# Optimization experiments

Measured on AMD Instinct MI355X. Metric: run time of the kernel, lower is better.

The kernel has to match this reference:

```python
import jax, jax.numpy as jnp
import numpy as np

B, S, D, E = 4, 4096, 1024, 8

def setup_inputs() -> dict:
    key = jax.random.key(0)
    k1, k2, k3, k4, k5 = jax.random.split(key, 5)
    scale = 1.0 / np.sqrt(D)
    return {
        "x": jax.random.normal(k1, (B, S, D), dtype=jnp.float32),
        "Wg": jax.random.normal(k2, (D, D), dtype=jnp.float32) * scale,   # gate Linear(D, D)
        "bg": jnp.zeros((D,), dtype=jnp.float32),
        "We": jax.random.normal(k3, (E, D, D), dtype=jnp.float32) * scale,  # per-expert Linear(D, D)
        "be": jnp.zeros((E, D), dtype=jnp.float32),
    }

def reference(x, Wg, bg, We, be):
    # gating network: Linear + Softmax over last dim (size D, per the original module)
    probs = jax.nn.softmax(x @ Wg + bg, axis=-1)           # [B,S,D]
    idx = jnp.argmax(probs, axis=-1)                        # [B,S], values in [0, D)
    p = jnp.take_along_axis(probs, idx[..., None], axis=-1)[..., 0]  # top-1 gate prob
    e_idx = idx % We.shape[0]                               # map argmax to expert id
    # run every expert densely, then select routed expert per token (top-1 switch routing)
    h = jax.nn.relu(jnp.einsum('bsd,edf->besf', x, We) + be[None, :, None, :])  # [B,E,S,D]
    onehot = jax.nn.one_hot(e_idx, We.shape[0], dtype=x.dtype)                   # [B,S,E]
    out = jnp.einsum('besf,bse->bsf', h, onehot) * p[..., None]                  # [B,S,D]
    return out
```

## Files before the change

kernel.cpp:

```cpp
#include <hip/hip_runtime.h>
#include <stdint.h>
#include <stddef.h>

#define TOK    16384
#define DDIM   1024
#define NEXP   8
#define BMT    128
#define RB_MAX 136
#define MARGIN 2.5e-2f
#define AMBIG_CAP 4096
#define BK     64

typedef __bf16 bf16x8 __attribute__((ext_vector_type(8)));
typedef float  f32x4  __attribute__((ext_vector_type(4)));
typedef unsigned short u16x8 __attribute__((ext_vector_type(8)));

__device__ __forceinline__ unsigned short f2bf(float f) {
    unsigned int u = __float_as_uint(f);
    u += 0x7fff + ((u >> 16) & 1);
    return (unsigned short)(u >> 16);
}

__device__ __forceinline__ void gload_lds16(const void* g, void* l) {
    __builtin_amdgcn_global_load_lds(
        (const __attribute__((address_space(1))) unsigned int*)g,
        (__attribute__((address_space(3))) unsigned int*)l, 16, 0, 0);
}

__global__ __launch_bounds__(256) void cvt_x(
    const float* __restrict__ x, unsigned short* __restrict__ xbf)
{
    const size_t t = ((size_t)blockIdx.x * 256 + threadIdx.x) * 8;
    const float4 v0 = *(const float4*)(x + t);
    const float4 v1 = *(const float4*)(x + t + 4);
    const float vv[8] = {v0.x, v0.y, v0.z, v0.w, v1.x, v1.y, v1.z, v1.w};
    u16x8 hh;
#pragma unroll
    for (int j = 0; j < 8; j++) hh[j] = f2bf(vv[j]);
    *(u16x8*)(xbf + t) = hh;
}

__global__ __launch_bounds__(256) void transpose_mat(
    const float* __restrict__ src0, unsigned short* __restrict__ dst0)
{
    __shared__ float tile[32][33];
    const int e  = blockIdx.z;
    const int k0 = blockIdx.x * 32;
    const int n0 = blockIdx.y * 32;
    const int tx = threadIdx.x;
    const int ty = threadIdx.y;
    const float* src = src0 + (size_t)e * DDIM * DDIM;
    unsigned short* dst = dst0 + (size_t)e * DDIM * DDIM;
#pragma unroll
    for (int r = 0; r < 4; r++)
        tile[ty + r * 8][tx] = src[(size_t)(k0 + ty + r * 8) * DDIM + n0 + tx];
    __syncthreads();
#pragma unroll
    for (int r = 0; r < 4; r++)
        dst[(size_t)(n0 + ty + r * 8) * DDIM + k0 + tx] = f2bf(tile[tx][ty + r * 8]);
}

__global__ __launch_bounds__(256) void transpose_f32(
    const float* __restrict__ src, float* __restrict__ dst)
{
    __shared__ float tile[32][33];
    const int k0 = blockIdx.x * 32;
    const int n0 = blockIdx.y * 32;
    const int tx = threadIdx.x;
    const int ty = threadIdx.y;
#pragma unroll
    for (int r = 0; r < 4; r++)
        tile[ty + r * 8][tx] = src[(size_t)(k0 + ty + r * 8) * DDIM + n0 + tx];
    __syncthreads();
#pragma unroll
    for (int r = 0; r < 4; r++)
        dst[(size_t)(n0 + ty + r * 8) * DDIM + k0 + tx] = tile[tx][ty + r * 8];
}

__global__ __launch_bounds__(256) void gating_mfma(
    const unsigned short* __restrict__ xbf,
    const unsigned short* __restrict__ WgT,
    const float* __restrict__ bg, float* __restrict__ logits)
{
    __shared__ unsigned short Asm[128 * BK];
    __shared__ unsigned short Bsm[128 * BK];
    const int rb = blockIdx.x;
    const int nb = blockIdx.y;
    const int tid  = threadIdx.x;
    const int lane = tid & 63;
    const int wave = tid >> 6;
    const int q    = lane >> 4;
    const int m16  = lane & 15;
    const int wrow = (wave & 1) * 64;
    const int wcol = (wave >> 1) * 64;

    const unsigned short* Ag = xbf + (size_t)rb * 128 * DDIM;
    const unsigned short* Bg = WgT + (size_t)nb * 128 * DDIM;

    const unsigned short* pa[4];
    const unsigned short* pb[4];
#pragma unroll
    for (int i = 0; i < 4; i++) {
        const int idx = tid + i * 256;
        const int r = idx >> 3;
        const int c = idx & 7;
        const int g = (c ^ (r & 7)) * 8;
        pa[i] = Ag + (size_t)r * DDIM + g;
        pb[i] = Bg + (size_t)r * DDIM + g;
    }

    f32x4 acc[4][4];
#pragma unroll
    for (int i = 0; i < 4; i++)
#pragma unroll
        for (int j = 0; j < 4; j++) acc[i][j] = (f32x4){0.f, 0.f, 0.f, 0.f};

    for (int k0 = 0; k0 < DDIM; k0 += BK) {
#pragma unroll
        for (int i = 0; i < 4; i++) {
            gload_lds16(pa[i] + k0, &Asm[(tid + i * 256) * 8]);
            gload_lds16(pb[i] + k0, &Bsm[(tid + i * 256) * 8]);
        }
        __syncthreads();
#pragma unroll
        for (int s = 0; s < 2; s++) {
            const int cs = (((s << 2) + q) ^ (m16 & 7)) << 3;
            bf16x8 af[4], bfr[4];
#pragma unroll
            for (int i = 0; i < 4; i++)
                af[i] = *(const bf16x8*)&Asm[(wrow + i * 16 + m16) * BK + cs];
#pragma unroll
            for (int j = 0; j < 4; j++)
                bfr[j] = *(const bf16x8*)&Bsm[(wcol + j * 16 + m16) * BK + cs];
#pragma unroll
            for (int i = 0; i < 4; i++)
#pragma unroll
                for (int j = 0; j < 4; j++)
                    acc[i][j] = __builtin_amdgcn_mfma_f32_16x16x32_bf16(
                        af[i], bfr[j], acc[i][j], 0, 0, 0);
        }
        __syncthreads();
    }

    float bgv[4];
#pragma unroll
    for (int j = 0; j < 4; j++) bgv[j] = bg[nb * 128 + wcol + j * 16 + m16];
#pragma unroll
    for (int i = 0; i < 4; i++)
#pragma unroll
        for (int r = 0; r < 4; r++) {
            const int row = rb * 128 + wrow + i * 16 + q * 4 + r;
#pragma unroll
            for (int j = 0; j < 4; j++) {
                const int col = nb * 128 + wcol + j * 16 + m16;
                logits[(size_t)row * DDIM + col] = acc[i][j][r] + bgv[j];
            }
        }
}

__global__ __launch_bounds__(256) void row_stats(
    const float* __restrict__ logits, float* __restrict__ pout,
    int* __restrict__ eout, float* __restrict__ rmax_a, float* __restrict__ s_a,
    int* __restrict__ ambig, int* __restrict__ n_ambig)
{
    const int row  = blockIdx.x * 4 + (threadIdx.x >> 6);
    const int lane = threadIdx.x & 63;
    const float* L = logits + (size_t)row * DDIM;
    float vals[16];
#pragma unroll
    for (int i = 0; i < 4; i++)
        *(float4*)&vals[i * 4] = *(const float4*)&L[lane * 16 + i * 4];
    float m = vals[0]; int mi = lane * 16;
#pragma unroll
    for (int i = 1; i < 16; i++)
        if (vals[i] > m) { m = vals[i]; mi = lane * 16 + i; }
    for (int off = 32; off > 0; off >>= 1) {
        float ov = __shfl_down(m, off, 64);
        int   oi = __shfl_down(mi, off, 64);
        if (ov > m || (ov == m && oi < mi)) { m = ov; mi = oi; }
    }
    m  = __shfl(m, 0, 64);
    mi = __shfl(mi, 0, 64);
    float s = 0.f;
    int   c = 0;
#pragma unroll
    for (int i = 0; i < 16; i++) {
        s += expf(vals[i] - m);
        if (vals[i] >= m - MARGIN) c++;
    }
    for (int off = 32; off > 0; off >>= 1) {
        s += __shfl_xor(s, off, 64);
        c += __shfl_xor(c, off, 64);
    }
    if (lane == 0) {
        pout[row] = 1.0f / s;
        eout[row] = mi & (NEXP - 1);
        rmax_a[row] = m;
        s_a[row] = s;
        if (c > 1) {
            int k = atomicAdd(n_ambig, 1);
            if (k < AMBIG_CAP) ambig[k] = row;
        }
    }
}

__global__ __launch_bounds__(64) void fixup(
    const float* __restrict__ logits, const float* __restrict__ x,
    const float* __restrict__ WgTf, const float* __restrict__ bg,
    const float* __restrict__ rmax_a, const float* __restrict__ s_a,
    const int* __restrict__ ambig, const int* __restrict__ n_ambig,
    int* __restrict__ eout, float* __restrict__ pout)
{
    int n = *n_ambig; if (n > AMBIG_CAP) n = AMBIG_CAP;
    if ((int)blockIdx.x >= n) return;
    const int row  = ambig[blockIdx.x];
    const int lane = threadIdx.x;
    const float rmax = rmax_a[row];
    const float* L = logits + (size_t)row * DDIM;
    __shared__ int scnt;
    __shared__ int scol[32];
    if (lane == 0) scnt = 0;
    __syncthreads();
    for (int j = lane; j < DDIM; j += 64)
        if (L[j] >= rmax - MARGIN) {
            int k = atomicAdd(&scnt, 1);
            if (k < 32) scol[k] = j;
        }
    __syncthreads();
    int ncand = scnt < 32 ? scnt : 32;
    double bestv = -1e300; int bestc = DDIM;
    for (int cidx = 0; cidx < ncand; cidx++) {
        const int col = scol[cidx];
        const float* Wcol = WgTf + (size_t)col * DDIM;
        double s = 0.0;
        for (int k = lane; k < DDIM; k += 64)
            s += (double)x[(size_t)row * DDIM + k] * (double)Wcol[k];
        for (int off = 32; off > 0; off >>= 1) s += __shfl_down(s, off, 64);
        s = __shfl(s, 0, 64);
        s += (double)bg[col];
        if (s > bestv || (s == bestv && col < bestc)) { bestv = s; bestc = col; }
    }
    if (lane == 0) {
        eout[row] = bestc & (NEXP - 1);
        pout[row] = expf(L[bestc] - rmax) / s_a[row];
    }
}

__global__ __launch_bounds__(256) void histo(const int* __restrict__ eout,
                                             int* __restrict__ cnt)
{
    __shared__ int h[NEXP];
    if (threadIdx.x < NEXP) h[threadIdx.x] = 0;
    __syncthreads();
    const int t = blockIdx.x * 256 + threadIdx.x;
    if (t < TOK) atomicAdd(&h[eout[t]], 1);
    __syncthreads();
    if (threadIdx.x < NEXP) atomicAdd(&cnt[threadIdx.x], h[threadIdx.x]);
}

__global__ __launch_bounds__(256) void compute_offsets(
    const int* __restrict__ cnt, int* __restrict__ start,
    int* __restrict__ blk_expert)
{
    const int tid = threadIdx.x;
    int st[NEXP + 1];
    int total = 0;
#pragma unroll
    for (int e = 0; e < NEXP; e++) {
        st[e] = total;
        total += ((cnt[e] + BMT - 1) / BMT) * BMT;
    }
    st[NEXP] = total;
    if (tid <= NEXP) start[tid] = st[tid];
    if (tid < RB_MAX) {
        const int s = tid * BMT;
        int ex = -1;
#pragma unroll
        for (int e = 0; e < NEXP; e++)
            if (s >= st[e] && s < st[e + 1]) ex = e;
        blk_expert[tid] = ex;
    }
}

__global__ __launch_bounds__(256) void assign_slots(
    const int* __restrict__ eout, const int* __restrict__ start,
    int* __restrict__ cursor, int* __restrict__ row_of_slot)
{
    __shared__ int h[NEXP];
    __shared__ int base[NEXP];
    const int tid = threadIdx.x;
    if (tid < NEXP) h[tid] = 0;
    __syncthreads();
    const int t = blockIdx.x * 256 + tid;
    int e = 0, lr = 0;
    if (t < TOK) {
        e = eout[t];
        lr = atomicAdd(&h[e], 1);
    }
    __syncthreads();
    if (tid < NEXP && h[tid] > 0)
        base[tid] = atomicAdd(&cursor[tid], h[tid]);
    __syncthreads();
    if (t < TOK)
        row_of_slot[start[e] + base[e] + lr] = t;
}

__global__ __launch_bounds__(256) void expert_gemm(
    const unsigned short* __restrict__ xbf, const unsigned short* __restrict__ WeT,
    const float* __restrict__ be, const float* __restrict__ p,
    const int* __restrict__ row_of_slot, const int* __restrict__ blk_expert,
    float* __restrict__ out)
{
    __shared__ unsigned short Asm[128 * BK];
    __shared__ unsigned short Bsm[128 * BK];
    __shared__ int rs[128];
    const int rb = blockIdx.x;
    const int nb = blockIdx.y;
    const int e = blk_expert[rb];
    if (e < 0) return;

    const int tid  = threadIdx.x;
    const int lane = tid & 63;
    const int wave = tid >> 6;
    const int q    = lane >> 4;
    const int m16  = lane & 15;
    const int wrow = (wave & 1) * 64;
    const int wcol = (wave >> 1) * 64;

    if (tid < 128) rs[tid] = row_of_slot[rb * 128 + tid];
    __syncthreads();

    const unsigned short* Bglob = WeT + (size_t)e * DDIM * DDIM + (size_t)nb * 128 * DDIM;

    const unsigned short* pa[4];
    const unsigned short* pb[4];
#pragma unroll
    for (int i = 0; i < 4; i++) {
        const int idx = tid + i * 256;
        const int r = idx >> 3;
        const int c = idx & 7;
        const int g = (c ^ (r & 7)) * 8;
        int tr = rs[r]; if (tr < 0) tr = 0;
        pa[i] = xbf + (size_t)tr * DDIM + g;
        pb[i] = Bglob + (size_t)r * DDIM + g;
    }

    f32x4 acc[4][4];
#pragma unroll
    for (int i = 0; i < 4; i++)
#pragma unroll
        for (int j = 0; j < 4; j++) acc[i][j] = (f32x4){0.f, 0.f, 0.f, 0.f};

    for (int k0 = 0; k0 < DDIM; k0 += BK) {
#pragma unroll
        for (int i = 0; i < 4; i++) {
            gload_lds16(pa[i] + k0, &Asm[(tid + i * 256) * 8]);
            gload_lds16(pb[i] + k0, &Bsm[(tid + i * 256) * 8]);
        }
        __syncthreads();
#pragma unroll
        for (int s = 0; s < 2; s++) {
            const int cs = (((s << 2) + q) ^ (m16 & 7)) << 3;
            bf16x8 af[4], bfr[4];
#pragma unroll
            for (int i = 0; i < 4; i++)
                af[i] = *(const bf16x8*)&Asm[(wrow + i * 16 + m16) * BK + cs];
#pragma unroll
            for (int j = 0; j < 4; j++)
                bfr[j] = *(const bf16x8*)&Bsm[(wcol + j * 16 + m16) * BK + cs];
#pragma unroll
            for (int i = 0; i < 4; i++)
#pragma unroll
                for (int j = 0; j < 4; j++)
                    acc[i][j] = __builtin_amdgcn_mfma_f32_16x16x32_bf16(
                        af[i], bfr[j], acc[i][j], 0, 0, 0);
        }
        __syncthreads();
    }

    float bev[4];
#pragma unroll
    for (int j = 0; j < 4; j++) bev[j] = be[e * DDIM + nb * 128 + wcol + j * 16 + m16];
#pragma unroll
    for (int i = 0; i < 4; i++)
#pragma unroll
        for (int r = 0; r < 4; r++) {
            const int t = rs[wrow + i * 16 + q * 4 + r];
            if (t < 0) continue;
            const float pv = p[t];
#pragma unroll
            for (int j = 0; j < 4; j++) {
                const int n = nb * 128 + wcol + j * 16 + m16;
                float v = acc[i][j][r] + bev[j];
                v = v > 0.f ? v : 0.f;
                out[(size_t)t * DDIM + n] = v * pv;
            }
        }
}

extern "C" void kernel_launch(void* const* d_in, const int* in_sizes, int n_in,
                              void* d_out, int out_size, void* d_ws, size_t ws_size,
                              hipStream_t stream)
{
    const float* x  = (const float*)d_in[0];
    const float* Wg = (const float*)d_in[1];
    const float* bg = (const float*)d_in[2];
    const float* We = (const float*)d_in[3];
    const float* be = (const float*)d_in[4];
    float* out = (float*)d_out;

    char* ws = (char*)d_ws;
    float* logits = (float*)ws;                 ws += (size_t)TOK * DDIM * 4;
    unsigned short* WeT = (unsigned short*)ws;  ws += (size_t)NEXP * DDIM * DDIM * 2;
    unsigned short* WgT = (unsigned short*)ws;  ws += (size_t)DDIM * DDIM * 2;
    float* WgTf = (float*)ws;                   ws += (size_t)DDIM * DDIM * 4;
    unsigned short* xbf = (unsigned short*)ws;  ws += (size_t)TOK * DDIM * 2;
    float* p = (float*)ws;                      ws += (size_t)TOK * 4;
    int* e_arr = (int*)ws;                      ws += (size_t)TOK * 4;
    float* rmax_a = (float*)ws;                 ws += (size_t)TOK * 4;
    float* s_a = (float*)ws;                    ws += (size_t)TOK * 4;
    int* row_of_slot = (int*)ws;                ws += (size_t)RB_MAX * BMT * 4;
    int* cnt = (int*)ws;                        ws += NEXP * 4;
    int* cursor = (int*)ws;                     ws += NEXP * 4;
    int* start = (int*)ws;                      ws += (NEXP + 1) * 4;
    int* blk_expert = (int*)ws;                 ws += RB_MAX * 4;
    int* ambig = (int*)ws;                      ws += AMBIG_CAP * 4;
    int* n_ambig = (int*)ws;                    ws += 4;

    hipMemsetAsync(cnt, 0, NEXP * 4, stream);
    hipMemsetAsync(cursor, 0, NEXP * 4, stream);
    hipMemsetAsync(n_ambig, 0, 4, stream);
    hipMemsetAsync(row_of_slot, 0xFF, (size_t)RB_MAX * BMT * 4, stream);

    cvt_x<<<TOK * DDIM / (256 * 8), 256, 0, stream>>>(x, xbf);
    transpose_mat<<<dim3(32, 32, 1), dim3(32, 8), 0, stream>>>(Wg, WgT);
    transpose_f32<<<dim3(32, 32), dim3(32, 8), 0, stream>>>(Wg, WgTf);
    transpose_mat<<<dim3(32, 32, NEXP), dim3(32, 8), 0, stream>>>(We, WeT);
    gating_mfma<<<dim3(TOK / 128, DDIM / 128), 256, 0, stream>>>(xbf, WgT, bg, logits);
    row_stats<<<TOK / 4, 256, 0, stream>>>(logits, p, e_arr, rmax_a, s_a, ambig, n_ambig);
    fixup<<<AMBIG_CAP, 64, 0, stream>>>(logits, x, WgTf, bg, rmax_a, s_a, ambig, n_ambig, e_arr, p);
    histo<<<TOK / 256, 256, 0, stream>>>(e_arr, cnt);
    compute_offsets<<<1, 256, 0, stream>>>(cnt, start, blk_expert);
    assign_slots<<<TOK / 256, 256, 0, stream>>>(e_arr, start, cursor, row_of_slot);
    expert_gemm<<<dim3(RB_MAX, DDIM / 128), 256, 0, stream>>>(
        xbf, WeT, be, p, row_of_slot, blk_expert, out);
}
```

Before: 326.1 us.

## Double-buffer GEMM K loop with 256x256 tiles and 512-thread blocks

```diff
diff --git a/kernel.cpp b/kernel.cpp
--- a/kernel.cpp
+++ b/kernel.cpp
@@ -5,11 +5,12 @@
 #define TOK    16384
 #define DDIM   1024
 #define NEXP   8
-#define BMT    128
-#define RB_MAX 136
+#define BMT    256
+#define RB_MAX 72
 #define MARGIN 2.5e-2f
 #define AMBIG_CAP 4096
-#define BK     64
+#define BK     32
+#define KT_N   (DDIM / BK)
 
 typedef __bf16 bf16x8 __attribute__((ext_vector_type(8)));
 typedef float  f32x4  __attribute__((ext_vector_type(4)));
@@ -26,6 +27,33 @@
         (const __attribute__((address_space(1))) unsigned int*)g,
         (__attribute__((address_space(3))) unsigned int*)l, 16, 0, 0);
 }
+
+#define BARX() do { __builtin_amdgcn_sched_barrier(0); \
+                    __builtin_amdgcn_s_barrier(); \
+                    __builtin_amdgcn_sched_barrier(0); } while (0)
+#define WAIT_VM4() do { asm volatile("s_waitcnt vmcnt(4)" ::: "memory"); \
+                        __builtin_amdgcn_sched_barrier(0); } while (0)
+#define WAIT_VM0() do { asm volatile("s_waitcnt vmcnt(0)" ::: "memory"); \
+                        __builtin_amdgcn_sched_barrier(0); } while (0)
+
+#define STAGE(bi, kt) do { const int _ko = (kt) * BK; \
+    _Pragma("unroll") for (int _i = 0; _i < 2; _i++) { \
+        gload_lds16(pa[_i] + _ko, &Asm[bi][(tid + _i * 512) * 8]); \
+        gload_lds16(pb[_i] + _ko, &Bsm[bi][(tid + _i * 512) * 8]); } } while (0)
+
+#define COMPUTE(b) do { \
+    const int cs = ((q ^ (m16 & 3)) << 3); \
+    bf16x8 af[8], bfr[4]; \
+    _Pragma("unroll") for (int _i = 0; _i < 8; _i++) \
+        af[_i] = *(const bf16x8*)&Asm[b][(wrow + _i * 16 + m16) * BK + cs]; \
+    _Pragma("unroll") for (int _j = 0; _j < 4; _j++) \
+        bfr[_j] = *(const bf16x8*)&Bsm[b][(wcol + _j * 16 + m16) * BK + cs]; \
+    __builtin_amdgcn_s_setprio(1); \
+    _Pragma("unroll") for (int _i = 0; _i < 8; _i++) \
+        _Pragma("unroll") for (int _j = 0; _j < 4; _j++) \
+            acc[_i][_j] = __builtin_amdgcn_mfma_f32_16x16x32_bf16( \
+                af[_i], bfr[_j], acc[_i][_j], 0, 0, 0); \
+    __builtin_amdgcn_s_setprio(0); } while (0)
 
 __global__ __launch_bounds__(256) void cvt_x(
     const float* __restrict__ x, unsigned short* __restrict__ xbf)
@@ -77,13 +105,13 @@
         dst[(size_t)(n0 + ty + r * 8) * DDIM + k0 + tx] = tile[tx][ty + r * 8];
 }
 
-__global__ __launch_bounds__(256) void gating_mfma(
+__global__ __launch_bounds__(512) void gating_mfma(
     const unsigned short* __restrict__ xbf,
     const unsigned short* __restrict__ WgT,
     const float* __restrict__ bg, float* __restrict__ logits)
 {
-    __shared__ unsigned short Asm[128 * BK];
-    __shared__ unsigned short Bsm[128 * BK];
+    __shared__ unsigned short Asm[2][256 * BK];
+    __shared__ unsigned short Bsm[2][256 * BK];
     const int rb = blockIdx.x;
     const int nb = blockIdx.y;
     const int tid  = threadIdx.x;
@@ -91,68 +119,58 @@
     const int wave = tid >> 6;
     const int q    = lane >> 4;
     const int m16  = lane & 15;
-    const int wrow = (wave & 1) * 64;
+    const int wrow = (wave & 1) * 128;
     const int wcol = (wave >> 1) * 64;
 
-    const unsigned short* Ag = xbf + (size_t)rb * 128 * DDIM;
-    const unsigned short* Bg = WgT + (size_t)nb * 128 * DDIM;
-
-    const unsigned short* pa[4];
-    const unsigned short* pb[4];
-#pragma unroll
-    for (int i = 0; i < 4; i++) {
-        const int idx = tid + i * 256;
-        const int r = idx >> 3;
-        const int c = idx & 7;
-        const int g = (c ^ (r & 7)) * 8;
+    const unsigned short* Ag = xbf + (size_t)rb * 256 * DDIM;
+    const unsigned short* Bg = WgT + (size_t)nb * 256 * DDIM;
+
+    const unsigned short* pa[2];
+    const unsigned short* pb[2];
+#pragma unroll
+    for (int i = 0; i < 2; i++) {
+        const int idx = tid + i * 512;
+        const int r = idx >> 2;
+        const int c = idx & 3;
+        const int g = (c ^ (r & 3)) * 8;
         pa[i] = Ag + (size_t)r * DDIM + g;
         pb[i] = Bg + (size_t)r * DDIM + g;
     }
 
-    f32x4 acc[4][4];
-#pragma unroll
-    for (int i = 0; i < 4; i++)
+    f32x4 acc[8][4];
+#pragma unroll
+    for (int i = 0; i < 8; i++)
 #pragma unroll
         for (int j = 0; j < 4; j++) acc[i][j] = (f32x4){0.f, 0.f, 0.f, 0.f};
 
-    for (int k0 = 0; k0 < DDIM; k0 += BK) {
-#pragma unroll
-        for (int i = 0; i < 4; i++) {
-            gload_lds16(pa[i] + k0, &Asm[(tid + i * 256) * 8]);
-            gload_lds16(pb[i] + k0, &Bsm[(tid + i * 256) * 8]);
-        }
-        __syncthreads();
-#pragma unroll
-        for (int s = 0; s < 2; s++) {
-            const int cs = (((s << 2) + q) ^ (m16 & 7)) << 3;
-            bf16x8 af[4], bfr[4];
-#pragma unroll
-            for (int i = 0; i < 4; i++)
-                af[i] = *(const bf16x8*)&Asm[(wrow + i * 16 + m16) * BK + cs];
-#pragma unroll
-            for (int j = 0; j < 4; j++)
-                bfr[j] = *(const bf16x8*)&Bsm[(wcol + j * 16 + m16) * BK + cs];
-#pragma unroll
-            for (int i = 0; i < 4; i++)
-#pragma unroll
-                for (int j = 0; j < 4; j++)
-                    acc[i][j] = __builtin_amdgcn_mfma_f32_16x16x32_bf16(
-                        af[i], bfr[j], acc[i][j], 0, 0, 0);
-        }
-        __syncthreads();
-    }
+    STAGE(0, 0);
+    STAGE(1, 1);
+    WAIT_VM4(); BARX();
+
+#pragma unroll 1
+    for (int it = 0; it < (KT_N - 2) / 2; ++it) {
+        COMPUTE(0); BARX();
+        STAGE(0, 2 * it + 2);
+        WAIT_VM4(); BARX();
+        COMPUTE(1); BARX();
+        STAGE(1, 2 * it + 3);
+        WAIT_VM4(); BARX();
+    }
+    COMPUTE(0); BARX();
+    WAIT_VM0(); BARX();
+    COMPUTE(1);
 
     float bgv[4];
 #pragma unroll
-    for (int j = 0; j < 4; j++) bgv[j] = bg[nb * 128 + wcol + j * 16 + m16];
-#pragma unroll
-    for (int i = 0; i < 4; i++)
+    for (int j = 0; j < 4; j++) bgv[j] = bg[nb * 256 + wcol + j * 16 + m16];
+#pragma unroll
+    for (int i = 0; i < 8; i++)
 #pragma unroll
         for (int r = 0; r < 4; r++) {
-            const int row = rb * 128 + wrow + i * 16 + q * 4 + r;
+            const int row = rb * 256 + wrow + i * 16 + q * 4 + r;
 #pragma unroll
             for (int j = 0; j < 4; j++) {
-                const int col = nb * 128 + wcol + j * 16 + m16;
+                const int col = nb * 256 + wcol + j * 16 + m16;
                 logits[(size_t)row * DDIM + col] = acc[i][j][r] + bgv[j];
             }
         }
@@ -305,15 +323,14 @@
         row_of_slot[start[e] + base[e] + lr] = t;
 }
 
-__global__ __launch_bounds__(256) void expert_gemm(
+__global__ __launch_bounds__(512) void expert_gemm(
     const unsigned short* __restrict__ xbf, const unsigned short* __restrict__ WeT,
     const float* __restrict__ be, const float* __restrict__ p,
     const int* __restrict__ row_of_slot, const int* __restrict__ blk_expert,
     float* __restrict__ out)
 {
-    __shared__ unsigned short Asm[128 * BK];
-    __shared__ unsigned short Bsm[128 * BK];
-    __shared__ int rs[128];
+    __shared__ unsigned short Asm[2][256 * BK];
+    __shared__ unsigned short Bsm[2][256 * BK];
     const int rb = blockIdx.x;
     const int nb = blockIdx.y;
     const int e = blk_expert[rb];
@@ -324,73 +341,61 @@
     const int wave = tid >> 6;
     const int q    = lane >> 4;
     const int m16  = lane & 15;
-    const int wrow = (wave & 1) * 64;
+    const int wrow = (wave & 1) * 128;
     const int wcol = (wave >> 1) * 64;
 
-    if (tid < 128) rs[tid] = row_of_slot[rb * 128 + tid];
-    __syncthreads();
-
-    const unsigned short* Bglob = WeT + (size_t)e * DDIM * DDIM + (size_t)nb * 128 * DDIM;
-
-    const unsigned short* pa[4];
-    const unsigned short* pb[4];
-#pragma unroll
-    for (int i = 0; i < 4; i++) {
-        const int idx = tid + i * 256;
-        const int r = idx >> 3;
-        const int c = idx & 7;
-        const int g = (c ^ (r & 7)) * 8;
-        int tr = rs[r]; if (tr < 0) tr = 0;
+    const int* rsg = row_of_slot + rb * 256;
+    const unsigned short* Bglob = WeT + (size_t)e * DDIM * DDIM + (size_t)nb * 256 * DDIM;
+
+    const unsigned short* pa[2];
+    const unsigned short* pb[2];
+#pragma unroll
+    for (int i = 0; i < 2; i++) {
+        const int idx = tid + i * 512;
+        const int r = idx >> 2;
+        const int c = idx & 3;
+        const int g = (c ^ (r & 3)) * 8;
+        int tr = rsg[r]; if (tr < 0) tr = 0;
         pa[i] = xbf + (size_t)tr * DDIM + g;
         pb[i] = Bglob + (size_t)r * DDIM + g;
     }
 
-    f32x4 acc[4][4];
-#pragma unroll
-    for (int i = 0; i < 4; i++)
+    f32x4 acc[8][4];
+#pragma unroll
+    for (int i = 0; i < 8; i++)
 #pragma unroll
         for (int j = 0; j < 4; j++) acc[i][j] = (f32x4){0.f, 0.f, 0.f, 0.f};
 
-    for (int k0 = 0; k0 < DDIM; k0 += BK) {
-#pragma unroll
-        for (int i = 0; i < 4; i++) {
-            gload_lds16(pa[i] + k0, &Asm[(tid + i * 256) * 8]);
-            gload_lds16(pb[i] + k0, &Bsm[(tid + i * 256) * 8]);
-        }
-        __syncthreads();
-#pragma unroll
-        for (int s = 0; s < 2; s++) {
-            const int cs = (((s << 2) + q) ^ (m16 & 7)) << 3;
-            bf16x8 af[4], bfr[4];
-#pragma unroll
-            for (int i = 0; i < 4; i++)
-                af[i] = *(const bf16x8*)&Asm[(wrow + i * 16 + m16) * BK + cs];
-#pragma unroll
-            for (int j = 0; j < 4; j++)
-                bfr[j] = *(const bf16x8*)&Bsm[(wcol + j * 16 + m16) * BK + cs];
-#pragma unroll
-            for (int i = 0; i < 4; i++)
-#pragma unroll
-                for (int j = 0; j < 4; j++)
-                    acc[i][j] = __builtin_amdgcn_mfma_f32_16x16x32_bf16(
-                        af[i], bfr[j], acc[i][j], 0, 0, 0);
-        }
-        __syncthreads();
-    }
+    STAGE(0, 0);
+    STAGE(1, 1);
+    WAIT_VM4(); BARX();
+
+#pragma unroll 1
+    for (int it = 0; it < (KT_N - 2) / 2; ++it) {
+        COMPUTE(0); BARX();
+        STAGE(0, 2 * it + 2);
+        WAIT_VM4(); BARX();
+        COMPUTE(1); BARX();
+        STAGE(1, 2 * it + 3);
+        WAIT_VM4(); BARX();
+    }
+    COMPUTE(0); BARX();
+    WAIT_VM0(); BARX();
+    COMPUTE(1);
 
     float bev[4];
 #pragma unroll
-    for (int j = 0; j < 4; j++) bev[j] = be[e * DDIM + nb * 128 + wcol + j * 16 + m16];
-#pragma unroll
-    for (int i = 0; i < 4; i++)
+    for (int j = 0; j < 4; j++) bev[j] = be[e * DDIM + nb * 256 + wcol + j * 16 + m16];
+#pragma unroll
+    for (int i = 0; i < 8; i++)
 #pragma unroll
         for (int r = 0; r < 4; r++) {
-            const int t = rs[wrow + i * 16 + q * 4 + r];
+            const int t = rsg[wrow + i * 16 + q * 4 + r];
             if (t < 0) continue;
             const float pv = p[t];
 #pragma unroll
             for (int j = 0; j < 4; j++) {
-                const int n = nb * 128 + wcol + j * 16 + m16;
+                const int n = nb * 256 + wcol + j * 16 + m16;
                 float v = acc[i][j][r] + bev[j];
                 v = v > 0.f ? v : 0.f;
                 out[(size_t)t * DDIM + n] = v * pv;
@@ -436,12 +441,12 @@
     transpose_mat<<<dim3(32, 32, 1), dim3(32, 8), 0, stream>>>(Wg, WgT);
     transpose_f32<<<dim3(32, 32), dim3(32, 8), 0, stream>>>(Wg, WgTf);
     transpose_mat<<<dim3(32, 32, NEXP), dim3(32, 8), 0, stream>>>(We, WeT);
-    gating_mfma<<<dim3(TOK / 128, DDIM / 128), 256, 0, stream>>>(xbf, WgT, bg, logits);
+    gating_mfma<<<dim3(TOK / 256, DDIM / 256), 512, 0, stream>>>(xbf, WgT, bg, logits);
     row_stats<<<TOK / 4, 256, 0, stream>>>(logits, p, e_arr, rmax_a, s_a, ambig, n_ambig);
     fixup<<<AMBIG_CAP, 64, 0, stream>>>(logits, x, WgTf, bg, rmax_a, s_a, ambig, n_ambig, e_arr, p);
     histo<<<TOK / 256, 256, 0, stream>>>(e_arr, cnt);
     compute_offsets<<<1, 256, 0, stream>>>(cnt, start, blk_expert);
     assign_slots<<<TOK / 256, 256, 0, stream>>>(e_arr, start, cursor, row_of_slot);
-    expert_gemm<<<dim3(RB_MAX, DDIM / 128), 256, 0, stream>>>(
+    expert_gemm<<<dim3(RB_MAX, DDIM / 256), 512, 0, stream>>>(
         xbf, WeT, be, p, row_of_slot, blk_expert, out);
 }
```

New measurement: 342.1 us. 4.9% more time.
